# Kernel tuning notes

Measured on AMD Instinct MI355X. Metric: run time of the kernel, lower is better.

## Reference

```python
import jax, jax.numpy as jnp
import numpy as np

S = 16384   # num src nodes
D = 16384   # num dst nodes
FS = 128    # src feature len
FD = 128    # dst feature len
R = 50.0    # dist threshold (m)
L = 2005.0  # box side so avg degree ~ 32
LN_EPS = 1e-5


def setup_inputs() -> dict:
    rng = np.random.default_rng(0)
    src_pos_np = rng.uniform(0.0, L, (S, 2)).astype(np.float32)
    dst_pos_np = rng.uniform(0.0, L, (D, 2)).astype(np.float32)
    # radius-graph edge construction (data-dependent, done once outside jit)
    es, ed = [], []
    CH = 2048
    for i in range(0, S, CH):
        d = np.linalg.norm(src_pos_np[i:i + CH, None, :] - dst_pos_np[None, :, :], axis=-1)
        si, di = np.nonzero(d <= R)
        es.append((si + i).astype(np.int32))
        ed.append(di.astype(np.int32))
    edge_src_idx = jnp.asarray(np.concatenate(es))
    edge_dst_idx = jnp.asarray(np.concatenate(ed))

    key = jax.random.key(0)
    ks = jax.random.split(key, 12)
    w = lambda k, shape: (jax.random.normal(k, shape, jnp.float32) * 0.02)
    return {
        'src_node_features': jax.random.normal(ks[0], (S, FS), jnp.float32),
        'src_node_pos': jnp.asarray(src_pos_np),
        'dst_node_features': jax.random.normal(ks[1], (D, FD), jnp.float32),
        'dst_node_pos': jnp.asarray(dst_pos_np),
        'src_w': w(ks[2], (FS, FS)), 'src_b': jnp.zeros((FS,), jnp.float32),
        'dst_w': w(ks[3], (FD, FD)), 'dst_b': jnp.zeros((FD,), jnp.float32),
        'dist_w': w(ks[4], (2, FD)), 'dist_b': jnp.zeros((FD,), jnp.float32),
        'edge_w1': w(ks[5], (FS + FD + FD, FD)), 'edge_b1': jnp.zeros((FD,), jnp.float32),
        'edge_w2': w(ks[6], (FD, FD)), 'edge_b2': jnp.zeros((FD,), jnp.float32),
        'ln_g': jnp.ones((FD,), jnp.float32), 'ln_b': jnp.zeros((FD,), jnp.float32),
        'out_w': w(ks[7], (FD, FD)), 'out_b': jnp.zeros((FD,), jnp.float32),
        'edge_src_idx': edge_src_idx,
        'edge_dst_idx': edge_dst_idx,
    }


def reference(src_node_features, src_node_pos, dst_node_features, dst_node_pos,
              src_w, src_b, dst_w, dst_b, dist_w, dist_b,
              edge_w1, edge_b1, edge_w2, edge_b2, ln_g, ln_b, out_w, out_b,
              edge_src_idx, edge_dst_idx):
    # node encoders: Linear + ReLU
    src_enc = jax.nn.relu(src_node_features @ src_w + src_b)   # [S, FS]
    dst_enc = jax.nn.relu(dst_node_features @ dst_w + dst_b)   # [D, FD]
    # gather per-edge
    e_src = src_enc[edge_src_idx]                               # [E, FS]
    e_dst = dst_enc[edge_dst_idx]                               # [E, FD]
    e_dpos = src_node_pos[edge_src_idx] - dst_node_pos[edge_dst_idx]  # [E, 2]
    e_dist = jax.nn.relu(e_dpos @ dist_w + dist_b)              # [E, FD]
    # edge MLP: Linear-ReLU-Linear on concat [E, FS+FD+FD]
    e_in = jnp.concatenate([e_src, e_dist, e_dst], axis=-1)
    e_out = jax.nn.relu(e_in @ edge_w1 + edge_b1) @ edge_w2 + edge_b2  # [E, FD]
    # scatter-add to destination nodes
    agg = dst_enc + jax.ops.segment_sum(e_out, edge_dst_idx, num_segments=D)
    # LayerNorm + ReLU + Linear + residual + ReLU
    mu = jnp.mean(agg, axis=-1, keepdims=True)
    var = jnp.mean(jnp.square(agg - mu), axis=-1, keepdims=True)
    ln = (agg - mu) * jax.lax.rsqrt(var + LN_EPS) * ln_g + ln_b
    h = jax.nn.relu(ln) @ out_w + out_b + dst_node_features
    return jax.nn.relu(h)
```

## Files before the change

kernel.cpp:

```cpp
#include <hip/hip_runtime.h>

typedef unsigned short ushort_t;
typedef unsigned int uint_t;
typedef short bhalf8 __attribute__((ext_vector_type(8)));
typedef float f32x4 __attribute__((ext_vector_type(4)));
typedef float f32x2 __attribute__((ext_vector_type(2)));

#define DEG_CAP 96

__device__ __forceinline__ float b2f(ushort_t u) {
    union { uint_t i; float f; } v; v.i = ((uint_t)u) << 16; return v.f;
}
__device__ __forceinline__ float u2f(uint_t u) {
    union { uint_t i; float f; } v; v.i = u; return v.f;
}
__device__ __forceinline__ ushort_t f2b(float f) {
    union { float f; uint_t i; } v; v.f = f;
    uint_t r = v.i + 0x7fffu + ((v.i >> 16) & 1u);
    return (ushort_t)(r >> 16);
}
__device__ __forceinline__ uint_t f2u(float f) {
    union { float f; uint_t i; } v; v.f = f; return v.i;
}
__device__ __forceinline__ uint_t pack_trunc(float lo, float hi) {
    return (f2u(lo) >> 16) | (f2u(hi) & 0xffff0000u);
}
__device__ __forceinline__ uint_t pack_rhu(float lo, float hi) {
    return ((f2u(lo) + 0x8000u) >> 16) | ((f2u(hi) + 0x8000u) & 0xffff0000u);
}
__device__ __forceinline__ uint_t addpack_trunc(uint_t a, uint_t b) {
    f32x2 A, B;
    A.x = u2f(a << 16); A.y = u2f(a & 0xffff0000u);
    B.x = u2f(b << 16); B.y = u2f(b & 0xffff0000u);
    f32x2 C = A + B;
    return pack_trunc(C.x, C.y);
}

__global__ __launch_bounds__(256) void prep_kernel(
    const float* __restrict__ wsrc, const float* __restrict__ wdst,
    const float* __restrict__ w2,   const float* __restrict__ wout,
    const float* __restrict__ w1,
    ushort_t* __restrict__ msrc, ushort_t* __restrict__ mdst,
    ushort_t* __restrict__ m2,   ushort_t* __restrict__ mout,
    ushort_t* __restrict__ m1a,  ushort_t* __restrict__ m1b,
    ushort_t* __restrict__ m1c,
    const int* __restrict__ esi, const int* __restrict__ edi, int E,
    int* __restrict__ deg, int* __restrict__ bucket,
    int2* __restrict__ edge_sd, int Epad,
    float* __restrict__ hsum, int countB, int zeroB, int Dn)
{
    int b = blockIdx.x, tid = threadIdx.x;
    if (b < 56) {
        const float* ins[7] = { wsrc, wdst, w2, wout, w1, w1 + 16384, w1 + 32768 };
        ushort_t* outs[7]   = { msrc, mdst, m2, mout, m1a, m1b, m1c };
        int mat = b >> 3;
        const float* in = ins[mat];
        ushort_t* out = outs[mat];
        int flat = (b & 7)*256 + tid;
        int nt = flat >> 8, rem = flat & 255;
        int ks = rem >> 6, lane = rem & 63;
        int q = lane >> 4, m = lane & 15;
        #pragma unroll
        for (int j = 0; j < 8; ++j)
            out[flat*8 + j] = f2b(in[(ks*32 + q*8 + j)*128 + nt*16 + m]);
    } else if (b < 56 + countB) {
        int i = (b - 56)*256 + tid;
        if (i < E) {
            int d = edi[i];
            int p = atomicAdd(&deg[d], 1);
            if (p < DEG_CAP) bucket[(size_t)d*DEG_CAP + p] = esi[i];
        }
    } else {
        int zb = b - 56 - countB;
        float4* h4 = (float4*)hsum;
        int total4 = Dn*32;
        for (int i = zb*256 + tid; i < total4; i += zeroB*256)
            h4[i] = make_float4(0.f, 0.f, 0.f, 0.f);
        uint2* e2 = (uint2*)edge_sd;
        for (int i = zb*256 + tid; i < Epad; i += zeroB*256)
            e2[i] = make_uint2(0u, 0xFFFFFFFFu);
    }
}

__global__ __launch_bounds__(256) void enc2_kernel(
    const float* __restrict__ src_feat, const float* __restrict__ dst_feat,
    const ushort_t* __restrict__ msrc, const ushort_t* __restrict__ mdst,
    const ushort_t* __restrict__ m1a,  const ushort_t* __restrict__ m1c,
    const float* __restrict__ src_b,   const float* __restrict__ dst_b,
    const float* __restrict__ b1,
    ushort_t* __restrict__ Csrc, ushort_t* __restrict__ Cdst,
    ushort_t* __restrict__ dst_enc,
    const int* __restrict__ deg, int* __restrict__ P,
    int Dn, int Sb, int Db)
{
    int tid = threadIdx.x, blk = blockIdx.x;

    if (blk == Sb + Db) {
        __shared__ int sums[256];
        int per = Dn >> 8;
        const int4* d4 = (const int4*)(deg + tid*per);
        int4 v[16]; int s = 0;
        #pragma unroll
        for (int k = 0; k < 16; ++k) {
            v[k] = d4[k];
            v[k].x = min(v[k].x, DEG_CAP); v[k].y = min(v[k].y, DEG_CAP);
            v[k].z = min(v[k].z, DEG_CAP); v[k].w = min(v[k].w, DEG_CAP);
            s += v[k].x + v[k].y + v[k].z + v[k].w;
        }
        sums[tid] = s;
        __syncthreads();
        for (int off = 1; off < 256; off <<= 1) {
            int x = (tid >= off) ? sums[tid - off] : 0;
            __syncthreads();
            sums[tid] += x;
            __syncthreads();
        }
        int run = sums[tid] - s;
        int4* n4 = (int4*)(P + tid*per);
        #pragma unroll
        for (int k = 0; k < 16; ++k) {
            int4 o;
            o.x = run; run += v[k].x;
            o.y = run; run += v[k].y;
            o.z = run; run += v[k].z;
            o.w = run; run += v[k].w;
            n4[k] = o;
        }
        return;
    }

    __shared__ ushort_t A_l[64*136];
    __shared__ ushort_t E_l[64*136];
    __shared__ float b_l[128];
    __shared__ float b2_l[128];

    const float* A; const ushort_t *W1m, *W2m; const float* bias; const float* bias2;
    ushort_t *outC, *outEnc; int rowbase;
    if (blk < Sb) { A = src_feat; W1m = msrc; W2m = m1a; bias = src_b;
                    outC = Csrc; outEnc = nullptr; rowbase = blk*64; bias2 = nullptr; }
    else          { A = dst_feat; W1m = mdst; W2m = m1c; bias = dst_b;
                    outC = Cdst; outEnc = dst_enc; rowbase = (blk - Sb)*64; bias2 = b1; }

    const float4* A4 = (const float4*)A;
    for (int i = tid; i < 2048; i += 256) {
        int r = i >> 5, c = i & 31;
        float4 v = A4[(size_t)(rowbase + r)*32 + c];
        uint2 u;
        u.x = pack_trunc(v.x, v.y);
        u.y = pack_trunc(v.z, v.w);
        *(uint2*)(A_l + r*136 + c*4) = u;
    }
    if (tid < 128) { b_l[tid] = bias[tid]; b2_l[tid] = bias2 ? bias2[tid] : 0.f; }
    __syncthreads();

    int lane = tid & 63, w = tid >> 6, q = lane >> 4, m = lane & 15;
    const bhalf8* Wv1 = (const bhalf8*)W1m;
    f32x4 acc[4][2] = {};
    #pragma unroll
    for (int ks = 0; ks < 4; ++ks) {
        bhalf8 bf0 = Wv1[((2*w)*4 + ks)*64 + lane];
        bhalf8 bf1 = Wv1[((2*w+1)*4 + ks)*64 + lane];
        #pragma unroll
        for (int mt = 0; mt < 4; ++mt) {
            bhalf8 a = *(const bhalf8*)(A_l + (mt*16 + m)*136 + ks*32 + q*8);
            acc[mt][0] = __builtin_amdgcn_mfma_f32_16x16x32_bf16(a, bf0, acc[mt][0], 0, 0, 0);
            acc[mt][1] = __builtin_amdgcn_mfma_f32_16x16x32_bf16(a, bf1, acc[mt][1], 0, 0, 0);
        }
    }
    #pragma unroll
    for (int mt = 0; mt < 4; ++mt)
    #pragma unroll
    for (int nt = 0; nt < 2; ++nt)
    #pragma unroll
    for (int reg = 0; reg < 4; ++reg) {
        int col = w*32 + nt*16 + m;
        int row = mt*16 + q*4 + reg;
        E_l[row*136 + col] = f2b(fmaxf(acc[mt][nt][reg] + b_l[col], 0.f));
    }
    __syncthreads();

    if (outEnc) {
        for (int i = tid; i < 1024; i += 256) {
            int r = i >> 4, c = i & 15;
            ((uint4*)outEnc)[(size_t)(rowbase + r)*16 + c] = *(const uint4*)(E_l + r*136 + c*8);
        }
    }

    const bhalf8* Wv2 = (const bhalf8*)W2m;
    f32x4 acc2[4][2] = {};
    #pragma unroll
    for (int ks = 0; ks < 4; ++ks) {
        bhalf8 bf0 = Wv2[((2*w)*4 + ks)*64 + lane];
        bhalf8 bf1 = Wv2[((2*w+1)*4 + ks)*64 + lane];
        #pragma unroll
        for (int mt = 0; mt < 4; ++mt) {
            bhalf8 a = *(const bhalf8*)(E_l + (mt*16 + m)*136 + ks*32 + q*8);
            acc2[mt][0] = __builtin_amdgcn_mfma_f32_16x16x32_bf16(a, bf0, acc2[mt][0], 0, 0, 0);
            acc2[mt][1] = __builtin_amdgcn_mfma_f32_16x16x32_bf16(a, bf1, acc2[mt][1], 0, 0, 0);
        }
    }
    #pragma unroll
    for (int mt = 0; mt < 4; ++mt)
    #pragma unroll
    for (int nt = 0; nt < 2; ++nt)
    #pragma unroll
    for (int reg = 0; reg < 4; ++reg) {
        int col = w*32 + nt*16 + m;
        int row = mt*16 + q*4 + reg;
        A_l[row*136 + col] = f2b(acc2[mt][nt][reg] + b2_l[col]);
    }
    __syncthreads();
    for (int i = tid; i < 1024; i += 256) {
        int r = i >> 4, c = i & 15;
        ((uint4*)outC)[(size_t)(rowbase + r)*16 + c] = *(const uint4*)(A_l + r*136 + c*8);
    }
}

__global__ __launch_bounds__(256) void csr_kernel(
    const int* __restrict__ P, const int* __restrict__ deg,
    const int* __restrict__ bucket, int2* __restrict__ edge_sd, int Dn)
{
    int t = blockIdx.x*256 + threadIdx.x;
    int d = t >> 2, pl = t & 3;
    if (d >= Dn) return;
    int st = P[d];
    int n = min(deg[d], DEG_CAP);
    const int* bk = bucket + (size_t)d*DEG_CAP;
    for (int p = pl; p < n; p += 4)
        edge_sd[st + p] = make_int2(bk[p], d);
}

__global__ __launch_bounds__(512, 8) void edge_kernel(
    const ushort_t* __restrict__ Csrc, const ushort_t* __restrict__ Cdst,
    const float* __restrict__ src_pos, const float* __restrict__ dst_pos,
    const int2* __restrict__ edge_sd, int E, int nTiles,
    const ushort_t* __restrict__ w1bm,
    const float* __restrict__ dist_w, const float* __restrict__ dist_b,
    float* __restrict__ hsum)
{
    __shared__ char pool[18432];
    __shared__ ushort_t G[64*136];
    __shared__ int segd[64];
    __shared__ ushort_t seg16[64];
    __shared__ float2 dxy_l[64];
    __shared__ float dw0_l[128], dw1_l[128], db_l[128];
    __shared__ int nseg_s;

    ushort_t* X  = (ushort_t*)pool;
    ushort_t* Hb = (ushort_t*)pool;

    int tid = threadIdx.x;

    int orig = blockIdx.x;
    int qq = nTiles >> 3, rr = nTiles & 7;
    int xcd = orig & 7, idx = orig >> 3;
    int blk = (xcd < rr ? xcd*(qq + 1) : rr*(qq + 1) + (xcd - rr)*qq) + idx;

    int lane = tid & 63, w = tid >> 6, q = lane >> 4, m = lane & 15;

    const bhalf8* Wv = (const bhalf8*)w1bm;
    bhalf8 wf0 = Wv[(w*4 + 0)*64 + lane];
    bhalf8 wf1 = Wv[(w*4 + 1)*64 + lane];
    bhalf8 wf2 = Wv[(w*4 + 2)*64 + lane];
    bhalf8 wf3 = Wv[(w*4 + 3)*64 + lane];

    int r0 = tid >> 4, c16 = tid & 15;
    const uint4* cs4 = (const uint4*)Csrc;
    const uint4* cd4 = (const uint4*)Cdst;
    int2 e0 = edge_sd[blk*64 + r0];
    int2 e1 = edge_sd[blk*64 + r0 + 32];
    uint4 ga0 = cs4[(size_t)e0.x*16 + c16];
    uint4 gb0 = cd4[(size_t)max(e0.y, 0)*16 + c16];
    uint4 ga1 = cs4[(size_t)e1.x*16 + c16];
    uint4 gb1 = cd4[(size_t)max(e1.y, 0)*16 + c16];

    if (tid < 128) {
        dw0_l[tid] = dist_w[tid];
        dw1_l[tid] = dist_w[128 + tid];
        db_l[tid]  = dist_b[tid];
    }

    if (tid < 64) {
        int2 sd = edge_sd[blk*64 + tid];
        int s = sd.x, d = sd.y;
        float dx = 0.f, dy = 0.f;
        if (d >= 0) {
            float2 sp = ((const float2*)src_pos)[s];
            float2 dp = ((const float2*)dst_pos)[d];
            dx = sp.x - dp.x; dy = sp.y - dp.y;
        }
        dxy_l[tid] = make_float2(dx, dy);
        int dprev = __shfl_up(d, 1);
        bool st = (tid == 0) || (d != dprev);
        unsigned long long smask = __ballot(st);
        int segreg = (int)__popcll(smask << (63 - tid)) - 1;
        seg16[tid] = (ushort_t)segreg;
        if (st) segd[segreg] = (d >= 0) ? d*128 : -1;
        if (tid == 0) nseg_s = (int)__popcll(smask);
    }
    __syncthreads();

    {
        int j2 = (tid & 63)*2;
        int rr2 = tid >> 6;
        float w00 = dw0_l[j2], w01 = dw0_l[j2+1];
        float w10 = dw1_l[j2], w11 = dw1_l[j2+1];
        float bb0 = db_l[j2],  bb1 = db_l[j2+1];
        #pragma unroll
        for (int k = 0; k < 8; ++k) {
            int r = rr2 + k*8;
            float2 dd = dxy_l[r];
            float v0 = fmaxf(fmaf(dd.x, w00, fmaf(dd.y, w10, bb0)), 0.f);
            float v1 = fmaxf(fmaf(dd.x, w01, fmaf(dd.y, w11, bb1)), 0.f);
            *(uint_t*)(X + r*136 + j2) = pack_trunc(v0, v1);
        }
    }

    {
        uint4 u;
        u.x = addpack_trunc(ga0.x, gb0.x);
        u.y = addpack_trunc(ga0.y, gb0.y);
        u.z = addpack_trunc(ga0.z, gb0.z);
        u.w = addpack_trunc(ga0.w, gb0.w);
        *(uint4*)(G + r0*136 + c16*8) = u;
        u.x = addpack_trunc(ga1.x, gb1.x);
        u.y = addpack_trunc(ga1.y, gb1.y);
        u.z = addpack_trunc(ga1.z, gb1.z);
        u.w = addpack_trunc(ga1.w, gb1.w);
        *(uint4*)(G + (r0 + 32)*136 + c16*8) = u;
    }
    __syncthreads();

    f32x4 acc[4] = {};
    #pragma unroll
    for (int mt = 0; mt < 4; ++mt) {
        bhalf8 a0 = *(const bhalf8*)(X + (mt*16 + m)*136 + 0*32 + q*8);
        acc[mt] = __builtin_amdgcn_mfma_f32_16x16x32_bf16(a0, wf0, acc[mt], 0, 0, 0);
        bhalf8 a1 = *(const bhalf8*)(X + (mt*16 + m)*136 + 1*32 + q*8);
        acc[mt] = __builtin_amdgcn_mfma_f32_16x16x32_bf16(a1, wf1, acc[mt], 0, 0, 0);
        bhalf8 a2 = *(const bhalf8*)(X + (mt*16 + m)*136 + 2*32 + q*8);
        acc[mt] = __builtin_amdgcn_mfma_f32_16x16x32_bf16(a2, wf2, acc[mt], 0, 0, 0);
        bhalf8 a3 = *(const bhalf8*)(X + (mt*16 + m)*136 + 3*32 + q*8);
        acc[mt] = __builtin_amdgcn_mfma_f32_16x16x32_bf16(a3, wf3, acc[mt], 0, 0, 0);
    }
    __syncthreads();

    int col = w*16 + m;
    #pragma unroll
    for (int mt = 0; mt < 4; ++mt) {
        int row0 = mt*16 + q*4;
        const ushort_t* gp = G + row0*136 + col;
        float v0 = fmaxf(acc[mt][0] + b2f(gp[0]),   0.f);
        float v1 = fmaxf(acc[mt][1] + b2f(gp[136]), 0.f);
        float v2 = fmaxf(acc[mt][2] + b2f(gp[272]), 0.f);
        float v3 = fmaxf(acc[mt][3] + b2f(gp[408]), 0.f);
        uint2 u;
        u.x = pack_rhu(v0, v1);
        u.y = pack_rhu(v2, v3);
        *(uint2*)(Hb + col*72 + row0) = u;
    }
    __builtin_amdgcn_sched_barrier(0);

    int ns = nseg_s;
    bhalf8 sv0 = *(const bhalf8*)(seg16 + q*8);
    bhalf8 sv1 = *(const bhalf8*)(seg16 + 32 + q*8);
    const ushort_t* hrow = Hb + col*72 + q*8;
    bhalf8 hb0 = *(const bhalf8*)(hrow);
    bhalf8 hb1 = *(const bhalf8*)(hrow + 32);
    const short onebf = (short)0x3f80;
    for (int sb = 0; sb*16 < ns; ++sb) {
        short target = (short)(sb*16 + m);
        bhalf8 a0, a1;
        #pragma unroll
        for (int j = 0; j < 8; ++j) {
            a0[j] = (sv0[j] == target) ? onebf : (short)0;
            a1[j] = (sv1[j] == target) ? onebf : (short)0;
        }
        f32x4 o = {};
        o = __builtin_amdgcn_mfma_f32_16x16x32_bf16(a0, hb0, o, 0, 0, 0);
        o = __builtin_amdgcn_mfma_f32_16x16x32_bf16(a1, hb1, o, 0, 0, 0);
        #pragma unroll
        for (int reg = 0; reg < 4; ++reg) {
            int seg = sb*16 + q*4 + reg;
            if (seg < ns) {
                int ofs = segd[seg];
                if (ofs >= 0) atomicAdd(&hsum[(size_t)ofs + col], o[reg]);
            }
        }
    }
}

__global__ __launch_bounds__(256) void aggfinal16_kernel(
    const float* __restrict__ hsum, const ushort_t* __restrict__ w2m,
    const float* __restrict__ b2, const int* __restrict__ deg,
    const ushort_t* __restrict__ dst_enc, const float* __restrict__ ln_g,
    const float* __restrict__ ln_b, const ushort_t* __restrict__ moutm,
    const float* __restrict__ out_b, const float* __restrict__ dst_feat,
    float* __restrict__ out)
{
    __shared__ ushort_t A_l[16*136];
    __shared__ ushort_t E2[16*136];
    __shared__ float ps[64], ps2[64];
    __shared__ float muv[16], invv[16];
    __shared__ float pb2[128], pg[128], plb[128], pob[128];
    __shared__ int dgl[16];

    int tid = threadIdx.x, blk = blockIdx.x;
    int lane = tid & 63, w = tid >> 6, q = lane >> 4, m = lane & 15;

    if (tid < 128) { pb2[tid] = b2[tid]; pg[tid] = ln_g[tid];
                     plb[tid] = ln_b[tid]; pob[tid] = out_b[tid]; }
    if (tid < 16) dgl[tid] = deg[blk*16 + tid];
    {
        int r = tid >> 4, c = tid & 15;
        const float4* hv4 = (const float4*)hsum;
        size_t base = (size_t)(blk*16 + r)*32 + c*2;
        float4 p0 = hv4[base], p1 = hv4[base + 1];
        uint4 u;
        u.x = pack_trunc(p0.x, p0.y);
        u.y = pack_trunc(p0.z, p0.w);
        u.z = pack_trunc(p1.x, p1.y);
        u.w = pack_trunc(p1.z, p1.w);
        *(uint4*)(A_l + r*136 + c*8) = u;
        *(uint4*)(E2 + r*136 + c*8) = ((const uint4*)dst_enc)[(size_t)(blk*16 + r)*16 + c];
    }
    __syncthreads();

    const bhalf8* Wv2 = (const bhalf8*)w2m;
    f32x4 acc[2] = {};
    #pragma unroll
    for (int ks = 0; ks < 4; ++ks) {
        bhalf8 bf0 = Wv2[((2*w)*4 + ks)*64 + lane];
        bhalf8 bf1 = Wv2[((2*w+1)*4 + ks)*64 + lane];
        bhalf8 a = *(const bhalf8*)(A_l + m*136 + ks*32 + q*8);
        acc[0] = __builtin_amdgcn_mfma_f32_16x16x32_bf16(a, bf0, acc[0], 0, 0, 0);
        acc[1] = __builtin_amdgcn_mfma_f32_16x16x32_bf16(a, bf1, acc[1], 0, 0, 0);
    }
    float y[2][4];
    #pragma unroll
    for (int nt = 0; nt < 2; ++nt)
    #pragma unroll
    for (int reg = 0; reg < 4; ++reg) {
        int col = w*32 + nt*16 + m;
        int rowl = q*4 + reg;
        y[nt][reg] = acc[nt][reg] + (float)dgl[rowl]*pb2[col] + b2f(E2[rowl*136 + col]);
    }
    float s[4], s2[4];
    #pragma unroll
    for (int reg = 0; reg < 4; ++reg) {
        s[reg]  = y[0][reg] + y[1][reg];
        s2[reg] = y[0][reg]*y[0][reg] + y[1][reg]*y[1][reg];
    }
    #pragma unroll
    for (int o = 1; o < 16; o <<= 1) {
        #pragma unroll
        for (int reg = 0; reg < 4; ++reg) {
            s[reg]  += __shfl_xor(s[reg],  o);
            s2[reg] += __shfl_xor(s2[reg], o);
        }
    }
    if (m == 0) {
        #pragma unroll
        for (int reg = 0; reg < 4; ++reg) {
            ps[(q*4 + reg)*4 + w]  = s[reg];
            ps2[(q*4 + reg)*4 + w] = s2[reg];
        }
    }
    __syncthreads();
    if (tid < 16) {
        float su = ps[tid*4] + ps[tid*4+1] + ps[tid*4+2] + ps[tid*4+3];
        float sq = ps2[tid*4] + ps2[tid*4+1] + ps2[tid*4+2] + ps2[tid*4+3];
        float mu = su / 128.f;
        float var = sq / 128.f - mu*mu;
        muv[tid] = mu;
        invv[tid] = 1.0f / sqrtf(var + 1e-5f);
    }
    __syncthreads();
    #pragma unroll
    for (int nt = 0; nt < 2; ++nt)
    #pragma unroll
    for (int reg = 0; reg < 4; ++reg) {
        int col = w*32 + nt*16 + m;
        int rowl = q*4 + reg;
        float v = (y[nt][reg] - muv[rowl])*invv[rowl]*pg[col] + plb[col];
        A_l[rowl*136 + col] = f2b(fmaxf(v, 0.f));
    }
    __syncthreads();

    const bhalf8* Wo = (const bhalf8*)moutm;
    f32x4 acc2[2] = {};
    #pragma unroll
    for (int ks = 0; ks < 4; ++ks) {
        bhalf8 bf0 = Wo[((2*w)*4 + ks)*64 + lane];
        bhalf8 bf1 = Wo[((2*w+1)*4 + ks)*64 + lane];
        bhalf8 a = *(const bhalf8*)(A_l + m*136 + ks*32 + q*8);
        acc2[0] = __builtin_amdgcn_mfma_f32_16x16x32_bf16(a, bf0, acc2[0], 0, 0, 0);
        acc2[1] = __builtin_amdgcn_mfma_f32_16x16x32_bf16(a, bf1, acc2[1], 0, 0, 0);
    }
    #pragma unroll
    for (int nt = 0; nt < 2; ++nt)
    #pragma unroll
    for (int reg = 0; reg < 4; ++reg) {
        int col = w*32 + nt*16 + m;
        size_t grow = (size_t)blk*16 + q*4 + reg;
        float v = acc2[nt][reg] + pob[col] + dst_feat[grow*128 + col];
        out[grow*128 + col] = fmaxf(v, 0.f);
    }
}

extern "C" void kernel_launch(void* const* d_in, const int* in_sizes, int n_in,
                              void* d_out, int out_size, void* d_ws, size_t ws_size,
                              hipStream_t stream)
{
    const float* src_feat = (const float*)d_in[0];
    const float* src_pos  = (const float*)d_in[1];
    const float* dst_feat = (const float*)d_in[2];
    const float* dst_pos  = (const float*)d_in[3];
    const float* src_w    = (const float*)d_in[4];
    const float* src_b    = (const float*)d_in[5];
    const float* dst_w    = (const float*)d_in[6];
    const float* dst_b    = (const float*)d_in[7];
    const float* dist_w   = (const float*)d_in[8];
    const float* dist_b   = (const float*)d_in[9];
    const float* w1       = (const float*)d_in[10];
    const float* b1       = (const float*)d_in[11];
    const float* w2       = (const float*)d_in[12];
    const float* b2       = (const float*)d_in[13];
    const float* ln_g     = (const float*)d_in[14];
    const float* ln_b     = (const float*)d_in[15];
    const float* out_w    = (const float*)d_in[16];
    const float* out_b    = (const float*)d_in[17];
    const int* esi        = (const int*)d_in[18];
    const int* edi        = (const int*)d_in[19];
    int E = in_sizes[18];
    int S = in_sizes[0] / 128;
    int D = in_sizes[2] / 128;
    int nTiles = (E + 63) / 64;
    int Epad = nTiles*64;

    char* ws = (char*)d_ws;
    size_t off = 0;
    auto alloc = [&](size_t bytes) { char* p = ws + off; off += (bytes + 511) & ~(size_t)511; return p; };
    ushort_t* Csrc    = (ushort_t*)alloc((size_t)S*128*2);
    ushort_t* Cdst    = (ushort_t*)alloc((size_t)D*128*2);
    ushort_t* dst_enc = (ushort_t*)alloc((size_t)D*128*2);
    float*    hsum    = (float*)   alloc((size_t)D*128*4);
    ushort_t* t_src   = (ushort_t*)alloc(128*128*2);
    ushort_t* t_dst   = (ushort_t*)alloc(128*128*2);
    ushort_t* t_w2    = (ushort_t*)alloc(128*128*2);
    ushort_t* t_out   = (ushort_t*)alloc(128*128*2);
    ushort_t* t_1a    = (ushort_t*)alloc(128*128*2);
    ushort_t* t_1b    = (ushort_t*)alloc(128*128*2);
    ushort_t* t_1c    = (ushort_t*)alloc(128*128*2);
    int*      deg     = (int*)     alloc((size_t)D*4);
    int*      P       = (int*)     alloc((size_t)D*4);
    int*      bucket  = (int*)     alloc((size_t)D*DEG_CAP*4);
    int2*     edge_sd = (int2*)    alloc((size_t)Epad*8);

    hipMemsetAsync(deg, 0, (size_t)D*4, stream);

    int countB = (E + 255)/256;
    int zeroB = 256;
    prep_kernel<<<56 + countB + zeroB, 256, 0, stream>>>(
        src_w, dst_w, w2, out_w, w1,
        t_src, t_dst, t_w2, t_out, t_1a, t_1b, t_1c,
        esi, edi, E, deg, bucket, edge_sd, Epad, hsum, countB, zeroB, D);

    int Sb = S/64, Db = D/64;
    enc2_kernel<<<Sb + Db + 1, 256, 0, stream>>>(
        src_feat, dst_feat, t_src, t_dst, t_1a, t_1c, src_b, dst_b, b1,
        Csrc, Cdst, dst_enc, deg, P, D, Sb, Db);

    csr_kernel<<<(D*4 + 255)/256, 256, 0, stream>>>(P, deg, bucket, edge_sd, D);

    edge_kernel<<<nTiles, 512, 0, stream>>>(
        Csrc, Cdst, src_pos, dst_pos, edge_sd, E, nTiles,
        t_1b, dist_w, dist_b, hsum);

    aggfinal16_kernel<<<D/16, 256, 0, stream>>>(
        hsum, t_w2, b2, deg, dst_enc, ln_g, ln_b,
        t_out, out_b, dst_feat, (float*)d_out);
}
```

Baseline: 198.0 us.

## Make edge kernel persistent over 8 tiles with prefetched gathers and precomputed deltas

Each edge_kernel block now processes eight consecutive 64-edge tiles, loading the weight fragments once and double-buffering the edge metadata so the next tile's feature gathers are issued while the current tile's MFMAs run. The csr_kernel now writes position deltas into a widened int4 edge record, which removes the per-tile position gathers. The G+bias add is folded into the accumulator through an identity-matrix MFMA, and bf16 packing uses v_perm. In exchange the grid has fewer blocks, so parallelism drops and the XCD-aware tile remap is gone, and the edge records double in size.

```diff
diff --git a/kernel.cpp b/kernel.cpp
--- a/kernel.cpp
+++ b/kernel.cpp
@@ -7,6 +7,7 @@
 typedef float f32x2 __attribute__((ext_vector_type(2)));
 
 #define DEG_CAP 96
+#define TPB_TILES 8
 
 __device__ __forceinline__ float b2f(ushort_t u) {
     union { uint_t i; float f; } v; v.i = ((uint_t)u) << 16; return v.f;
@@ -23,18 +24,19 @@
     union { float f; uint_t i; } v; v.f = f; return v.i;
 }
 __device__ __forceinline__ uint_t pack_trunc(float lo, float hi) {
-    return (f2u(lo) >> 16) | (f2u(hi) & 0xffff0000u);
+    return __builtin_amdgcn_perm(f2u(hi), f2u(lo), 0x07060302u);
 }
 __device__ __forceinline__ uint_t pack_rhu(float lo, float hi) {
-    return ((f2u(lo) + 0x8000u) >> 16) | ((f2u(hi) + 0x8000u) & 0xffff0000u);
+    return __builtin_amdgcn_perm(f2u(hi) + 0x8000u, f2u(lo) + 0x8000u, 0x07060302u);
 }
 __device__ __forceinline__ uint_t addpack_trunc(uint_t a, uint_t b) {
-    f32x2 A, B;
-    A.x = u2f(a << 16); A.y = u2f(a & 0xffff0000u);
-    B.x = u2f(b << 16); B.y = u2f(b & 0xffff0000u);
-    f32x2 C = A + B;
-    return pack_trunc(C.x, C.y);
-}
+    float lo = u2f(a << 16) + u2f(b << 16);
+    float hi = u2f(a & 0xffff0000u) + u2f(b & 0xffff0000u);
+    return __builtin_amdgcn_perm(f2u(hi), f2u(lo), 0x07060302u);
+}
+
+#define LGKM_BAR() do { asm volatile("s_waitcnt lgkmcnt(0)" ::: "memory"); \
+                        __builtin_amdgcn_s_barrier(); } while (0)
 
 __global__ __launch_bounds__(256) void prep_kernel(
     const float* __restrict__ wsrc, const float* __restrict__ wdst,
@@ -46,7 +48,7 @@
     ushort_t* __restrict__ m1c,
     const int* __restrict__ esi, const int* __restrict__ edi, int E,
     int* __restrict__ deg, int* __restrict__ bucket,
-    int2* __restrict__ edge_sd, int Epad,
+    int4* __restrict__ edge_sd, int Epad,
     float* __restrict__ hsum, int countB, int zeroB, int Dn)
 {
     int b = blockIdx.x, tid = threadIdx.x;
@@ -76,9 +78,8 @@
         int total4 = Dn*32;
         for (int i = zb*256 + tid; i < total4; i += zeroB*256)
             h4[i] = make_float4(0.f, 0.f, 0.f, 0.f);
-        uint2* e2 = (uint2*)edge_sd;
         for (int i = zb*256 + tid; i < Epad; i += zeroB*256)
-            e2[i] = make_uint2(0u, 0xFFFFFFFFu);
+            edge_sd[i] = make_int4(0, -1, 0, 0);
     }
 }
 
@@ -218,45 +219,61 @@
 
 __global__ __launch_bounds__(256) void csr_kernel(
     const int* __restrict__ P, const int* __restrict__ deg,
-    const int* __restrict__ bucket, int2* __restrict__ edge_sd, int Dn)
+    const int* __restrict__ bucket,
+    const float* __restrict__ src_pos, const float* __restrict__ dst_pos,
+    int4* __restrict__ edge_sd, int Dn)
 {
     int t = blockIdx.x*256 + threadIdx.x;
     int d = t >> 2, pl = t & 3;
     if (d >= Dn) return;
     int st = P[d];
     int n = min(deg[d], DEG_CAP);
+    float2 dp = ((const float2*)dst_pos)[d];
     const int* bk = bucket + (size_t)d*DEG_CAP;
-    for (int p = pl; p < n; p += 4)
-        edge_sd[st + p] = make_int2(bk[p], d);
+    for (int p = pl; p < n; p += 4) {
+        int s = bk[p];
+        float2 sp = ((const float2*)src_pos)[s];
+        edge_sd[st + p] = make_int4(s, d,
+                                    __float_as_int(sp.x - dp.x),
+                                    __float_as_int(sp.y - dp.y));
+    }
 }
 
 __global__ __launch_bounds__(512, 8) void edge_kernel(
     const ushort_t* __restrict__ Csrc, const ushort_t* __restrict__ Cdst,
-    const float* __restrict__ src_pos, const float* __restrict__ dst_pos,
-    const int2* __restrict__ edge_sd, int E, int nTiles,
+    const int4* __restrict__ edge_sd, int nTiles,
     const ushort_t* __restrict__ w1bm,
     const float* __restrict__ dist_w, const float* __restrict__ dist_b,
     float* __restrict__ hsum)
 {
     __shared__ char pool[18432];
     __shared__ ushort_t G[64*136];
-    __shared__ int segd[64];
-    __shared__ ushort_t seg16[64];
-    __shared__ float2 dxy_l[64];
+    __shared__ float2 dxy_l[2][64];
+    __shared__ int2  sd_l[2][64];
+    __shared__ int   segd[2][64];
+    __shared__ ushort_t seg16[2][64];
+    __shared__ int nseg_s[2];
     __shared__ float dw0_l[128], dw1_l[128], db_l[128];
-    __shared__ int nseg_s;
 
     ushort_t* X  = (ushort_t*)pool;
     ushort_t* Hb = (ushort_t*)pool;
 
     int tid = threadIdx.x;
-
-    int orig = blockIdx.x;
-    int qq = nTiles >> 3, rr = nTiles & 7;
-    int xcd = orig & 7, idx = orig >> 3;
-    int blk = (xcd < rr ? xcd*(qq + 1) : rr*(qq + 1) + (xcd - rr)*qq) + idx;
-
     int lane = tid & 63, w = tid >> 6, q = lane >> 4, m = lane & 15;
+    int r0 = tid >> 4, c16 = tid & 15;
+
+    int t0 = blockIdx.x * TPB_TILES;
+    if (t0 >= nTiles) return;
+    int tEnd = min(t0 + TPB_TILES, nTiles);
+
+    const uint4* cs4 = (const uint4*)Csrc;
+    const uint4* cd4 = (const uint4*)Cdst;
+
+    if (tid < 128) {
+        dw0_l[tid] = dist_w[tid];
+        dw1_l[tid] = dist_w[128 + tid];
+        db_l[tid]  = dist_b[tid];
+    }
 
     const bhalf8* Wv = (const bhalf8*)w1bm;
     bhalf8 wf0 = Wv[(w*4 + 0)*64 + lane];
@@ -264,129 +281,150 @@
     bhalf8 wf2 = Wv[(w*4 + 2)*64 + lane];
     bhalf8 wf3 = Wv[(w*4 + 3)*64 + lane];
 
-    int r0 = tid >> 4, c16 = tid & 15;
-    const uint4* cs4 = (const uint4*)Csrc;
-    const uint4* cd4 = (const uint4*)Cdst;
-    int2 e0 = edge_sd[blk*64 + r0];
-    int2 e1 = edge_sd[blk*64 + r0 + 32];
-    uint4 ga0 = cs4[(size_t)e0.x*16 + c16];
-    uint4 gb0 = cd4[(size_t)max(e0.y, 0)*16 + c16];
-    uint4 ga1 = cs4[(size_t)e1.x*16 + c16];
-    uint4 gb1 = cd4[(size_t)max(e1.y, 0)*16 + c16];
-
-    if (tid < 128) {
-        dw0_l[tid] = dist_w[tid];
-        dw1_l[tid] = dist_w[128 + tid];
-        db_l[tid]  = dist_b[tid];
-    }
-
+    int p_id = (w & 1)*16;
+    int win = (w >> 1)*32;
+    bhalf8 iden;
+    #pragma unroll
+    for (int j = 0; j < 8; ++j)
+        iden[j] = (short)((q*8 + j == p_id + m) ? 0x3f80 : 0);
+
+    int4 recW;
+    uint4 ga0, gb0, ga1, gb1;
+    {
+        int4 re0 = edge_sd[(size_t)t0*64 + r0];
+        int4 re1 = edge_sd[(size_t)t0*64 + r0 + 32];
+        ga0 = cs4[(size_t)re0.x*16 + c16];
+        gb0 = cd4[(size_t)max(re0.y, 0)*16 + c16];
+        ga1 = cs4[(size_t)re1.x*16 + c16];
+        gb1 = cd4[(size_t)max(re1.y, 0)*16 + c16];
+    }
     if (tid < 64) {
-        int2 sd = edge_sd[blk*64 + tid];
-        int s = sd.x, d = sd.y;
-        float dx = 0.f, dy = 0.f;
-        if (d >= 0) {
-            float2 sp = ((const float2*)src_pos)[s];
-            float2 dp = ((const float2*)dst_pos)[d];
-            dx = sp.x - dp.x; dy = sp.y - dp.y;
-        }
-        dxy_l[tid] = make_float2(dx, dy);
+        int4 r = edge_sd[(size_t)t0*64 + tid];
+        dxy_l[0][tid] = make_float2(__int_as_float(r.z), __int_as_float(r.w));
+        sd_l[0][tid]  = make_int2(r.x, r.y);
+        int d = r.y;
         int dprev = __shfl_up(d, 1);
         bool st = (tid == 0) || (d != dprev);
         unsigned long long smask = __ballot(st);
         int segreg = (int)__popcll(smask << (63 - tid)) - 1;
-        seg16[tid] = (ushort_t)segreg;
-        if (st) segd[segreg] = (d >= 0) ? d*128 : -1;
-        if (tid == 0) nseg_s = (int)__popcll(smask);
-    }
-    __syncthreads();
-
-    {
-        int j2 = (tid & 63)*2;
-        int rr2 = tid >> 6;
-        float w00 = dw0_l[j2], w01 = dw0_l[j2+1];
-        float w10 = dw1_l[j2], w11 = dw1_l[j2+1];
-        float bb0 = db_l[j2],  bb1 = db_l[j2+1];
-        #pragma unroll
-        for (int k = 0; k < 8; ++k) {
-            int r = rr2 + k*8;
-            float2 dd = dxy_l[r];
-            float v0 = fmaxf(fmaf(dd.x, w00, fmaf(dd.y, w10, bb0)), 0.f);
-            float v1 = fmaxf(fmaf(dd.x, w01, fmaf(dd.y, w11, bb1)), 0.f);
-            *(uint_t*)(X + r*136 + j2) = pack_trunc(v0, v1);
-        }
-    }
-
-    {
-        uint4 u;
-        u.x = addpack_trunc(ga0.x, gb0.x);
-        u.y = addpack_trunc(ga0.y, gb0.y);
-        u.z = addpack_trunc(ga0.z, gb0.z);
-        u.w = addpack_trunc(ga0.w, gb0.w);
-        *(uint4*)(G + r0*136 + c16*8) = u;
-        u.x = addpack_trunc(ga1.x, gb1.x);
-        u.y = addpack_trunc(ga1.y, gb1.y);
-        u.z = addpack_trunc(ga1.z, gb1.z);
-        u.w = addpack_trunc(ga1.w, gb1.w);
-        *(uint4*)(G + (r0 + 32)*136 + c16*8) = u;
-    }
-    __syncthreads();
-
-    f32x4 acc[4] = {};
-    #pragma unroll
-    for (int mt = 0; mt < 4; ++mt) {
-        bhalf8 a0 = *(const bhalf8*)(X + (mt*16 + m)*136 + 0*32 + q*8);
-        acc[mt] = __builtin_amdgcn_mfma_f32_16x16x32_bf16(a0, wf0, acc[mt], 0, 0, 0);
-        bhalf8 a1 = *(const bhalf8*)(X + (mt*16 + m)*136 + 1*32 + q*8);
-        acc[mt] = __builtin_amdgcn_mfma_f32_16x16x32_bf16(a1, wf1, acc[mt], 0, 0, 0);
-        bhalf8 a2 = *(const bhalf8*)(X + (mt*16 + m)*136 + 2*32 + q*8);
-        acc[mt] = __builtin_amdgcn_mfma_f32_16x16x32_bf16(a2, wf2, acc[mt], 0, 0, 0);
-        bhalf8 a3 = *(const bhalf8*)(X + (mt*16 + m)*136 + 3*32 + q*8);
-        acc[mt] = __builtin_amdgcn_mfma_f32_16x16x32_bf16(a3, wf3, acc[mt], 0, 0, 0);
-    }
-    __syncthreads();
-
-    int col = w*16 + m;
-    #pragma unroll
-    for (int mt = 0; mt < 4; ++mt) {
-        int row0 = mt*16 + q*4;
-        const ushort_t* gp = G + row0*136 + col;
-        float v0 = fmaxf(acc[mt][0] + b2f(gp[0]),   0.f);
-        float v1 = fmaxf(acc[mt][1] + b2f(gp[136]), 0.f);
-        float v2 = fmaxf(acc[mt][2] + b2f(gp[272]), 0.f);
-        float v3 = fmaxf(acc[mt][3] + b2f(gp[408]), 0.f);
-        uint2 u;
-        u.x = pack_rhu(v0, v1);
-        u.y = pack_rhu(v2, v3);
-        *(uint2*)(Hb + col*72 + row0) = u;
-    }
-    __builtin_amdgcn_sched_barrier(0);
-
-    int ns = nseg_s;
-    bhalf8 sv0 = *(const bhalf8*)(seg16 + q*8);
-    bhalf8 sv1 = *(const bhalf8*)(seg16 + 32 + q*8);
-    const ushort_t* hrow = Hb + col*72 + q*8;
-    bhalf8 hb0 = *(const bhalf8*)(hrow);
-    bhalf8 hb1 = *(const bhalf8*)(hrow + 32);
-    const short onebf = (short)0x3f80;
-    for (int sb = 0; sb*16 < ns; ++sb) {
-        short target = (short)(sb*16 + m);
-        bhalf8 a0, a1;
-        #pragma unroll
-        for (int j = 0; j < 8; ++j) {
-            a0[j] = (sv0[j] == target) ? onebf : (short)0;
-            a1[j] = (sv1[j] == target) ? onebf : (short)0;
-        }
-        f32x4 o = {};
-        o = __builtin_amdgcn_mfma_f32_16x16x32_bf16(a0, hb0, o, 0, 0, 0);
-        o = __builtin_amdgcn_mfma_f32_16x16x32_bf16(a1, hb1, o, 0, 0, 0);
-        #pragma unroll
-        for (int reg = 0; reg < 4; ++reg) {
-            int seg = sb*16 + q*4 + reg;
-            if (seg < ns) {
-                int ofs = segd[seg];
-                if (ofs >= 0) atomicAdd(&hsum[(size_t)ofs + col], o[reg]);
+        seg16[0][tid] = (ushort_t)segreg;
+        if (st) segd[0][segreg] = (d >= 0) ? d*128 : -1;
+        if (tid == 0) nseg_s[0] = (int)__popcll(smask);
+        recW = edge_sd[(size_t)min(t0 + 1, nTiles - 1)*64 + tid];
+    }
+    LGKM_BAR();
+
+    int tb = 0;
+    for (int t = t0; t < tEnd; ++t) {
+        bool hasNext = (t + 1 < tEnd);
+
+        if (tid < 64 && hasNext) {
+            dxy_l[tb^1][tid] = make_float2(__int_as_float(recW.z), __int_as_float(recW.w));
+            sd_l[tb^1][tid]  = make_int2(recW.x, recW.y);
+            int d = recW.y;
+            int dprev = __shfl_up(d, 1);
+            bool st = (tid == 0) || (d != dprev);
+            unsigned long long smask = __ballot(st);
+            int segreg = (int)__popcll(smask << (63 - tid)) - 1;
+            seg16[tb^1][tid] = (ushort_t)segreg;
+            if (st) segd[tb^1][segreg] = (d >= 0) ? d*128 : -1;
+            if (tid == 0) nseg_s[tb^1] = (int)__popcll(smask);
+            recW = edge_sd[(size_t)min(t + 2, nTiles - 1)*64 + tid];
+        }
+        {
+            uint4 u;
+            u.x = addpack_trunc(ga0.x, gb0.x);
+            u.y = addpack_trunc(ga0.y, gb0.y);
+            u.z = addpack_trunc(ga0.z, gb0.z);
+            u.w = addpack_trunc(ga0.w, gb0.w);
+            *(uint4*)(G + r0*136 + c16*8) = u;
+            u.x = addpack_trunc(ga1.x, gb1.x);
+            u.y = addpack_trunc(ga1.y, gb1.y);
+            u.z = addpack_trunc(ga1.z, gb1.z);
+            u.w = addpack_trunc(ga1.w, gb1.w);
+            *(uint4*)(G + (r0 + 32)*136 + c16*8) = u;
+        }
+        {
+            int j2 = lane*2;
+            float w00 = dw0_l[j2], w01 = dw0_l[j2+1];
+            float w10 = dw1_l[j2], w11 = dw1_l[j2+1];
+            float bb0 = db_l[j2],  bb1 = db_l[j2+1];
+            #pragma unroll
+            for (int k = 0; k < 8; ++k) {
+                int r = w + k*8;
+                float2 dd = dxy_l[tb][r];
+                float v0 = fmaxf(fmaf(dd.x, w00, fmaf(dd.y, w10, bb0)), 0.f);
+                float v1 = fmaxf(fmaf(dd.x, w01, fmaf(dd.y, w11, bb1)), 0.f);
+                *(uint_t*)(X + r*136 + j2) = pack_trunc(v0, v1);
             }
         }
+        LGKM_BAR();
+
+        if (hasNext) {
+            int2 p0 = sd_l[tb^1][r0];
+            int2 p1 = sd_l[tb^1][r0 + 32];
+            ga0 = cs4[(size_t)p0.x*16 + c16];
+            gb0 = cd4[(size_t)max(p0.y, 0)*16 + c16];
+            ga1 = cs4[(size_t)p1.x*16 + c16];
+            gb1 = cd4[(size_t)max(p1.y, 0)*16 + c16];
+        }
+        f32x4 acc[4];
+        #pragma unroll
+        for (int mt = 0; mt < 4; ++mt) {
+            f32x4 z = {};
+            bhalf8 g = *(const bhalf8*)(G + (mt*16 + m)*136 + win + q*8);
+            acc[mt] = __builtin_amdgcn_mfma_f32_16x16x32_bf16(g, iden, z, 0, 0, 0);
+            bhalf8 a0 = *(const bhalf8*)(X + (mt*16 + m)*136 + 0*32 + q*8);
+            acc[mt] = __builtin_amdgcn_mfma_f32_16x16x32_bf16(a0, wf0, acc[mt], 0, 0, 0);
+            bhalf8 a1 = *(const bhalf8*)(X + (mt*16 + m)*136 + 1*32 + q*8);
+            acc[mt] = __builtin_amdgcn_mfma_f32_16x16x32_bf16(a1, wf1, acc[mt], 0, 0, 0);
+            bhalf8 a2 = *(const bhalf8*)(X + (mt*16 + m)*136 + 2*32 + q*8);
+            acc[mt] = __builtin_amdgcn_mfma_f32_16x16x32_bf16(a2, wf2, acc[mt], 0, 0, 0);
+            bhalf8 a3 = *(const bhalf8*)(X + (mt*16 + m)*136 + 3*32 + q*8);
+            acc[mt] = __builtin_amdgcn_mfma_f32_16x16x32_bf16(a3, wf3, acc[mt], 0, 0, 0);
+        }
+        LGKM_BAR();
+
+        int col = w*16 + m;
+        #pragma unroll
+        for (int mt = 0; mt < 4; ++mt) {
+            int row0 = mt*16 + q*4;
+            uint2 u;
+            u.x = pack_rhu(fmaxf(acc[mt][0], 0.f), fmaxf(acc[mt][1], 0.f));
+            u.y = pack_rhu(fmaxf(acc[mt][2], 0.f), fmaxf(acc[mt][3], 0.f));
+            *(uint2*)(Hb + col*72 + row0) = u;
+        }
+        __builtin_amdgcn_sched_barrier(0);
+
+        int ns = nseg_s[tb];
+        bhalf8 sv0 = *(const bhalf8*)(&seg16[tb][0] + q*8);
+        bhalf8 sv1 = *(const bhalf8*)(&seg16[tb][0] + 32 + q*8);
+        const ushort_t* hrow = Hb + col*72 + q*8;
+        bhalf8 hb0 = *(const bhalf8*)(hrow);
+        bhalf8 hb1 = *(const bhalf8*)(hrow + 32);
+        const short onebf = (short)0x3f80;
+        for (int sb = 0; sb*16 < ns; ++sb) {
+            short target = (short)(sb*16 + m);
+            bhalf8 a0, a1;
+            #pragma unroll
+            for (int j = 0; j < 8; ++j) {
+                a0[j] = (sv0[j] == target) ? onebf : (short)0;
+                a1[j] = (sv1[j] == target) ? onebf : (short)0;
+            }
+            f32x4 o = {};
+            o = __builtin_amdgcn_mfma_f32_16x16x32_bf16(a0, hb0, o, 0, 0, 0);
+            o = __builtin_amdgcn_mfma_f32_16x16x32_bf16(a1, hb1, o, 0, 0, 0);
+            #pragma unroll
+            for (int reg = 0; reg < 4; ++reg) {
+                int seg = sb*16 + q*4 + reg;
+                if (seg < ns) {
+                    int ofs = segd[tb][seg];
+                    if (ofs >= 0) atomicAdd(&hsum[(size_t)ofs + col], o[reg]);
+                }
+            }
+        }
+        LGKM_BAR();
+        tb ^= 1;
     }
 }
 
@@ -555,7 +593,7 @@
     int*      deg     = (int*)     alloc((size_t)D*4);
     int*      P       = (int*)     alloc((size_t)D*4);
     int*      bucket  = (int*)     alloc((size_t)D*DEG_CAP*4);
-    int2*     edge_sd = (int2*)    alloc((size_t)Epad*8);
+    int4*     edge_sd = (int4*)    alloc((size_t)Epad*16);
 
     hipMemsetAsync(deg, 0, (size_t)D*4, stream);
 
@@ -571,10 +609,12 @@
         src_feat, dst_feat, t_src, t_dst, t_1a, t_1c, src_b, dst_b, b1,
         Csrc, Cdst, dst_enc, deg, P, D, Sb, Db);
 
-    csr_kernel<<<(D*4 + 255)/256, 256, 0, stream>>>(P, deg, bucket, edge_sd, D);
-
-    edge_kernel<<<nTiles, 512, 0, stream>>>(
-        Csrc, Cdst, src_pos, dst_pos, edge_sd, E, nTiles,
+    csr_kernel<<<(D*4 + 255)/256, 256, 0, stream>>>(
+        P, deg, bucket, src_pos, dst_pos, edge_sd, D);
+
+    int nBlk = (nTiles + TPB_TILES - 1) / TPB_TILES;
+    edge_kernel<<<nBlk, 512, 0, stream>>>(
+        Csrc, Cdst, edge_sd, nTiles,
         t_1b, dist_w, dist_b, hsum);
 
     aggfinal16_kernel<<<D/16, 256, 0, stream>>>(
```

New measurement: 296.8 us. +49.9%, slower.
